# Optimization experiments

Hardware: AMD Instinct MI355X
Metric: run time of the kernel (lower is better)

The kernel has to match this reference:

```python
import jax, jax.numpy as jnp
import numpy as np

N_HEAD = 16

def _rope_cache(dim, T):
    # matches precompute_rope_cache: angles = outer(pos, 1/theta^(2i/dim))
    pos = jnp.arange(T, dtype=jnp.float32)
    freq = 1.0 / (10000.0 ** (jnp.arange(0, dim, 2, dtype=jnp.float32) / dim))
    ang = pos[:, None] * freq[None, :]  # (T, dim//2)
    return jnp.cos(ang), jnp.sin(ang)

def _apply_rope(x, cos, sin):
    # x: (B, H, T, hs). Faithful to the (nonstandard, roll-based) torch apply_rope,
    # including the reassignment of x_rot before it is used for x_pass.
    x_rot, x_pass = x[..., ::2], x[..., 1::2]
    c = cos[None, None]  # (1,1,T,hs//2)
    s = sin[None, None]
    new_rot = x_rot * c - jnp.roll(x_pass, 1, axis=-1) * s
    new_pass = x_pass * c + jnp.roll(new_rot, -1, axis=-1) * s
    return jnp.stack([new_rot, new_pass], axis=-1).reshape(x.shape)

def setup_inputs() -> dict:
    key = jax.random.key(0)
    k1, k2, k3 = jax.random.split(key, 3)
    B, T, C = 2, 2048, 1024
    x = jax.random.normal(k1, (B, T, C), dtype=jnp.float32)
    w_attn = jax.random.normal(k2, (3 * C, C), dtype=jnp.float32) * 0.02
    w_proj = jax.random.normal(k3, (C, C), dtype=jnp.float32) * 0.02
    return {"x": x, "w_attn": w_attn, "w_proj": w_proj}

def reference(x, w_attn, w_proj):
    B, T, C = x.shape
    H = N_HEAD
    hs = C // H
    qkv = jnp.einsum('btc,dc->btd', x, w_attn)  # fused QKV projection (no bias)
    q, k, v = jnp.split(qkv, 3, axis=-1)
    def heads(t):
        return t.reshape(B, T, H, hs).transpose(0, 2, 1, 3)  # (B,H,T,hs)
    q, k, v = heads(q), heads(k), heads(v)
    cos, sin = _rope_cache(hs, T)
    q = _apply_rope(q, cos, sin)
    k = _apply_rope(k, cos, sin)
    scores = jnp.einsum('bhqd,bhkd->bhqk', q, k) / jnp.sqrt(jnp.float32(hs))
    causal = jnp.tril(jnp.ones((T, T), dtype=bool))
    scores = jnp.where(causal[None, None], scores, -jnp.inf)
    att = jax.nn.softmax(scores, axis=-1)
    y = jnp.einsum('bhqk,bhkd->bhqd', att, v)
    y = y.transpose(0, 2, 1, 3).reshape(B, T, C)
    return jnp.einsum('btc,dc->btd', y, w_proj)
```

## Files before the change

kernel.cpp:

```cpp
#include <hip/hip_runtime.h>

#define T_SEQ 2048
#define NHEAD 16
#define HS 64

typedef __bf16 bf16x8 __attribute__((ext_vector_type(8)));
typedef float f32x4 __attribute__((ext_vector_type(4)));
typedef short short4v __attribute__((ext_vector_type(4)));

__device__ __forceinline__ unsigned short f2bf(float f) {
  union { float f; unsigned int u; } v; v.f = f;
  return (unsigned short)((v.u + 0x7fffu + ((v.u >> 16) & 1u)) >> 16);
}
__device__ __forceinline__ float bf2f(unsigned short h) {
  union { unsigned int u; float f; } v; v.u = ((unsigned int)h) << 16;
  return v.f;
}
__device__ __forceinline__ bf16x8 ld_bf8(const unsigned short* p) {
  return *(const bf16x8*)p;
}
__device__ __forceinline__ void st_bf8(unsigned short* p, bf16x8 v) {
  *(bf16x8*)p = v;
}
__device__ __forceinline__ bf16x8 cvt8(float4 a, float4 b) {
  bf16x8 r;
  r[0] = (__bf16)a.x; r[1] = (__bf16)a.y; r[2] = (__bf16)a.z; r[3] = (__bf16)a.w;
  r[4] = (__bf16)b.x; r[5] = (__bf16)b.y; r[6] = (__bf16)b.z; r[7] = (__bf16)b.w;
  return r;
}

__global__ __launch_bounds__(256, 2) void gemm_bt(
    const void* __restrict__ Av, const void* __restrict__ Bv,
    float* __restrict__ Cout,
    unsigned short* __restrict__ qb, unsigned short* __restrict__ kb,
    unsigned short* __restrict__ vtb,
    int M, int N, int K, int af32, int bf32, int mode) {
  __shared__ unsigned short As[128 * 64];
  __shared__ unsigned short Bs[128 * 64];
  const int tid = threadIdx.x;
  const int wid = tid >> 6, lane = tid & 63;
  const int quad = lane >> 4, l16 = lane & 15;
  const int m0 = blockIdx.y * 128, n0 = blockIdx.x * 128;
  const int wm = (wid >> 1) * 64, wn = (wid & 1) * 64;
  const int row_in = tid >> 3;
  const int col_in = (tid & 7) * 8;
  const float* Agf = (const float*)Av + (size_t)(m0 + row_in) * K + col_in;
  const float* Bgf = (const float*)Bv + (size_t)(n0 + row_in) * K + col_in;
  const unsigned short* Agh = (const unsigned short*)Av + (size_t)(m0 + row_in) * K + col_in;
  const unsigned short* Bgh = (const unsigned short*)Bv + (size_t)(n0 + row_in) * K + col_in;
  f32x4 acc[4][4] = {};
  const int nkt = K >> 6;
  for (int kt = 0; kt < nkt; ++kt) {
    bf16x8 as8[4], bs8[4];
    if (af32) {
      #pragma unroll
      for (int j = 0; j < 4; ++j) {
        const float* p = Agf + (size_t)j * 32 * K + kt * 64;
        as8[j] = cvt8(*(const float4*)p, *(const float4*)(p + 4));
      }
    } else {
      #pragma unroll
      for (int j = 0; j < 4; ++j)
        as8[j] = ld_bf8(Agh + (size_t)j * 32 * K + kt * 64);
    }
    if (bf32) {
      #pragma unroll
      for (int j = 0; j < 4; ++j) {
        const float* p = Bgf + (size_t)j * 32 * K + kt * 64;
        bs8[j] = cvt8(*(const float4*)p, *(const float4*)(p + 4));
      }
    } else {
      #pragma unroll
      for (int j = 0; j < 4; ++j)
        bs8[j] = ld_bf8(Bgh + (size_t)j * 32 * K + kt * 64);
    }
    __syncthreads();
    #pragma unroll
    for (int j = 0; j < 4; ++j) {
      st_bf8(&As[(j * 32 + row_in) * 64 + col_in], as8[j]);
      st_bf8(&Bs[(j * 32 + row_in) * 64 + col_in], bs8[j]);
    }
    __syncthreads();
    #pragma unroll
    for (int ks = 0; ks < 2; ++ks) {
      bf16x8 af[4], bfr[4];
      #pragma unroll
      for (int mt = 0; mt < 4; ++mt)
        af[mt] = ld_bf8(&As[(wm + mt * 16 + l16) * 64 + ks * 32 + quad * 8]);
      #pragma unroll
      for (int nt = 0; nt < 4; ++nt)
        bfr[nt] = ld_bf8(&Bs[(wn + nt * 16 + l16) * 64 + ks * 32 + quad * 8]);
      #pragma unroll
      for (int mt = 0; mt < 4; ++mt)
        #pragma unroll
        for (int nt = 0; nt < 4; ++nt)
          acc[mt][nt] = __builtin_amdgcn_mfma_f32_16x16x32_bf16(af[mt], bfr[nt], acc[mt][nt], 0, 0, 0);
    }
  }
  #pragma unroll
  for (int mt = 0; mt < 4; ++mt) {
    #pragma unroll
    for (int nt = 0; nt < 4; ++nt) {
      const int n = n0 + wn + nt * 16 + l16;
      #pragma unroll
      for (int r = 0; r < 4; ++r) {
        const int m = m0 + wm + mt * 16 + quad * 4 + r;
        if (mode == 0) {
          Cout[(size_t)m * N + n] = acc[mt][nt][r];
        } else {
          const unsigned short val = f2bf(acc[mt][nt][r]);
          const int b = m >> 11, t = m & (T_SEQ - 1);
          const int which = n >> 10, c = n & 1023;
          const int h = c >> 6, d = c & 63;
          const int bh = b * NHEAD + h;
          if (which == 0)      qb[((size_t)bh * T_SEQ + t) * HS + d] = val;
          else if (which == 1) kb[((size_t)bh * T_SEQ + t) * HS + d] = val;
          else                 vtb[((size_t)bh * HS + d) * T_SEQ + t] = val;
        }
      }
    }
  }
}

__global__ __launch_bounds__(256) void cvtbuf(const float* __restrict__ src,
                                              unsigned short* __restrict__ dst, int n) {
  const int i = (blockIdx.x * 256 + threadIdx.x) * 4;
  if (i < n) {
    const float4 v = *(const float4*)(src + i);
    ushort4 o;
    o.x = f2bf(v.x); o.y = f2bf(v.y); o.z = f2bf(v.z); o.w = f2bf(v.w);
    *(ushort4*)(dst + i) = o;
  }
}

__global__ __launch_bounds__(256, 1) void rope(unsigned short* __restrict__ qb,
                                               unsigned short* __restrict__ kb) {
  const int idx = blockIdx.x * 256 + threadIdx.x;
  const bool isq = idx < 65536;
  const float qs = isq ? 0.125f : 1.0f;
  unsigned short* buf = (isq ? qb : kb) + (size_t)(idx & 65535) * HS;
  const int t = idx & (T_SEQ - 1);
  float x[64];
  #pragma unroll
  for (int j = 0; j < 64; ++j) x[j] = bf2f(buf[j]);
  __asm__ volatile("" ::: "memory");
  float c[32], s[32], er[32];
  #pragma unroll
  for (int i = 0; i < 32; ++i) {
    const float ang = (float)t * exp2f(-0.41524101186092029f * (float)i);
    c[i] = cosf(ang); s[i] = sinf(ang);
  }
  #pragma unroll
  for (int i = 0; i < 32; ++i)
    er[i] = x[2 * i] * c[i] - x[(2 * i + 63) & 63] * s[i];
  #pragma unroll
  for (int i = 0; i < 32; ++i) {
    const float ep = x[2 * i + 1] * c[i] + er[(i + 1) & 31] * s[i];
    buf[2 * i]     = f2bf(er[i] * qs);
    buf[2 * i + 1] = f2bf(ep * qs);
  }
}

__global__ __launch_bounds__(64, 4) void attn(
    const unsigned short* __restrict__ qb, const unsigned short* __restrict__ kb,
    const unsigned short* __restrict__ vt, unsigned short* __restrict__ yb) {
  const int u = blockIdx.x;
  const int qi = 127 - (u >> 5);
  const int bh = u & 31;
  const int q0 = qi * 16;
  const int lane = threadIdx.x & 63;
  const int quad = lane >> 4, l16 = lane & 15;

  const unsigned short* qptr = qb + ((size_t)bh * T_SEQ + q0 + l16) * HS;
  const bf16x8 bq0 = ld_bf8(qptr + quad * 8);
  const bf16x8 bq1 = ld_bf8(qptr + 32 + quad * 8);

  f32x4 O[4] = {};
  float m_i = -1e30f, l_i = 0.f;

  const unsigned short* kbase = kb + (size_t)bh * T_SEQ * HS;
  const unsigned short* vbase = vt + (size_t)bh * HS * T_SEQ;
  const int nfull = (q0 >= 63) ? (((q0 - 63) >> 6) + 1) : 0;

  auto pass_body = [&](int k0, bool masked) {
    bf16x8 ak[4][2];
    #pragma unroll
    for (int t = 0; t < 4; ++t) {
      const unsigned short* kp = kbase + (size_t)(k0 + t * 16 + l16) * HS;
      ak[t][0] = ld_bf8(kp + quad * 8);
      ak[t][1] = ld_bf8(kp + 32 + quad * 8);
    }
    short4v vf[4][4];
    #pragma unroll
    for (int t = 0; t < 4; ++t)
      #pragma unroll
      for (int dg = 0; dg < 4; ++dg)
        vf[t][dg] = *(const short4v*)(vbase + (size_t)(dg * 16 + l16) * T_SEQ + k0 + t * 16 + quad * 4);
    f32x4 S[4] = {};
    #pragma unroll
    for (int t = 0; t < 4; ++t) {
      S[t] = __builtin_amdgcn_mfma_f32_16x16x32_bf16(ak[t][0], bq0, S[t], 0, 0, 0);
      S[t] = __builtin_amdgcn_mfma_f32_16x16x32_bf16(ak[t][1], bq1, S[t], 0, 0, 0);
    }
    float sv[16];
    #pragma unroll
    for (int t = 0; t < 4; ++t)
      #pragma unroll
      for (int r = 0; r < 4; ++r) {
        float v = S[t][r];
        if (masked) v = (k0 + t * 16 + quad * 4 + r <= q0 + l16) ? v : -1e30f;
        sv[t * 4 + r] = v;
      }
    float tm = sv[0];
    #pragma unroll
    for (int i = 1; i < 16; ++i) tm = fmaxf(tm, sv[i]);
    tm = fmaxf(tm, __shfl_xor(tm, 16, 64));
    tm = fmaxf(tm, __shfl_xor(tm, 32, 64));
    const float mnew = fmaxf(m_i, tm);
    const float alpha = __expf(m_i - mnew);
    float p[16], rs = 0.f;
    #pragma unroll
    for (int i = 0; i < 16; ++i) { p[i] = __expf(sv[i] - mnew); rs += p[i]; }
    rs += __shfl_xor(rs, 16, 64);
    rs += __shfl_xor(rs, 32, 64);
    l_i = l_i * alpha + rs;
    m_i = mnew;
    short4v pa[4];
    #pragma unroll
    for (int t = 0; t < 4; ++t) {
      short4v f;
      f[0] = (short)f2bf(p[t * 4 + 0]); f[1] = (short)f2bf(p[t * 4 + 1]);
      f[2] = (short)f2bf(p[t * 4 + 2]); f[3] = (short)f2bf(p[t * 4 + 3]);
      pa[t] = f;
    }
    float aD[4];
    #pragma unroll
    for (int r = 0; r < 4; ++r) aD[r] = __shfl(alpha, quad * 4 + r, 64);
    #pragma unroll
    for (int dg = 0; dg < 4; ++dg)
      #pragma unroll
      for (int r = 0; r < 4; ++r) O[dg][r] *= aD[r];
    #pragma unroll
    for (int t = 0; t < 4; ++t)
      #pragma unroll
      for (int dg = 0; dg < 4; ++dg)
        O[dg] = __builtin_amdgcn_mfma_f32_16x16x16bf16_1k(pa[t], vf[t][dg], O[dg], 0, 0, 0);
  };

  for (int k0 = 0; k0 < nfull * 64; k0 += 64) pass_body(k0, false);
  pass_body(nfull * 64, true);

  const int b = bh >> 4, h = bh & 15;
  float inv[4];
  #pragma unroll
  for (int r = 0; r < 4; ++r)
    inv[r] = 1.0f / fmaxf(__shfl(l_i, quad * 4 + r, 64), 1e-30f);
  #pragma unroll
  for (int r = 0; r < 4; ++r) {
    const int row = q0 + quad * 4 + r;
    #pragma unroll
    for (int dg = 0; dg < 4; ++dg)
      yb[((size_t)b * T_SEQ + row) * 1024 + h * HS + dg * 16 + l16] = f2bf(O[dg][r] * inv[r]);
  }
}

extern "C" void kernel_launch(void* const* d_in, const int* in_sizes, int n_in,
                              void* d_out, int out_size, void* d_ws, size_t ws_size,
                              hipStream_t stream) {
  const float* x      = (const float*)d_in[0];
  const float* w_attn = (const float*)d_in[1];
  const float* w_proj = (const float*)d_in[2];
  float* out = (float*)d_out;
  unsigned short* qb = (unsigned short*)d_ws;
  unsigned short* kb = qb + (size_t)4194304;
  unsigned short* vt = kb + (size_t)4194304;
  unsigned short* yb = vt + (size_t)4194304;

  if (ws_size >= (size_t)50331648 + (size_t)2097152) {
    unsigned short* xb  = yb + (size_t)4194304;
    unsigned short* wab = xb + (size_t)4194304;
    unsigned short* wpb = wab + (size_t)3145728;
    cvtbuf<<<dim3(4096), 256, 0, stream>>>(x, xb, 4194304);
    cvtbuf<<<dim3(3072), 256, 0, stream>>>(w_attn, wab, 3145728);
    cvtbuf<<<dim3(1024), 256, 0, stream>>>(w_proj, wpb, 1048576);
    gemm_bt<<<dim3(24, 32), 256, 0, stream>>>(xb, wab, nullptr, qb, kb, vt,
                                              4096, 3072, 1024, 0, 0, 1);
    rope<<<dim3(512), 256, 0, stream>>>(qb, kb);
    attn<<<dim3(4096), 64, 0, stream>>>(qb, kb, vt, yb);
    gemm_bt<<<dim3(8, 32), 256, 0, stream>>>(yb, wpb, out, nullptr, nullptr, nullptr,
                                             4096, 1024, 1024, 0, 0, 0);
  } else {
    gemm_bt<<<dim3(24, 32), 256, 0, stream>>>(x, w_attn, nullptr, qb, kb, vt,
                                              4096, 3072, 1024, 1, 1, 1);
    rope<<<dim3(512), 256, 0, stream>>>(qb, kb);
    attn<<<dim3(4096), 64, 0, stream>>>(qb, kb, vt, yb);
    gemm_bt<<<dim3(8, 32), 256, 0, stream>>>(yb, w_proj, out, nullptr, nullptr, nullptr,
                                             4096, 1024, 1024, 0, 1, 0);
  }
}
```

Measured before the change: 353.6 us.

## Split attention key loop across four waves per block with LDS merge

The attention kernel now launches 256 threads per block and distributes the 64-key tiles round-robin across four waves. Each wave keeps its own online-softmax state, and the partial results are merged in shared memory before wave 0 writes the normalized output. This is meant to shorten the serial per-block key loop for long causal rows and add latency hiding. In exchange it adds shared-memory use, a block barrier and merge work, and waves sit idle for short query rows.

```diff
diff --git a/kernel.cpp b/kernel.cpp
--- a/kernel.cpp
+++ b/kernel.cpp
@@ -161,13 +161,16 @@
   }
 }
 
-__global__ __launch_bounds__(64, 4) void attn(
+__global__ __launch_bounds__(256, 4) void attn(
     const unsigned short* __restrict__ qb, const unsigned short* __restrict__ kb,
     const unsigned short* __restrict__ vt, unsigned short* __restrict__ yb) {
+  __shared__ float Om[4][16][64];
+  __shared__ float Ml[4][2][16];
   const int u = blockIdx.x;
   const int qi = 127 - (u >> 5);
   const int bh = u & 31;
   const int q0 = qi * 16;
+  const int wid = threadIdx.x >> 6;
   const int lane = threadIdx.x & 63;
   const int quad = lane >> 4, l16 = lane & 15;
 
@@ -180,9 +183,11 @@
 
   const unsigned short* kbase = kb + (size_t)bh * T_SEQ * HS;
   const unsigned short* vbase = vt + (size_t)bh * HS * T_SEQ;
-  const int nfull = (q0 >= 63) ? (((q0 - 63) >> 6) + 1) : 0;
-
-  auto pass_body = [&](int k0, bool masked) {
+  const int P = (q0 + 16 + 63) >> 6;
+
+  for (int p = wid; p < P; p += 4) {
+    const int k0 = p * 64;
+    const bool masked = (p == P - 1);
     bf16x8 ak[4][2];
     #pragma unroll
     for (int t = 0; t < 4; ++t) {
@@ -218,9 +223,9 @@
     tm = fmaxf(tm, __shfl_xor(tm, 32, 64));
     const float mnew = fmaxf(m_i, tm);
     const float alpha = __expf(m_i - mnew);
-    float p[16], rs = 0.f;
-    #pragma unroll
-    for (int i = 0; i < 16; ++i) { p[i] = __expf(sv[i] - mnew); rs += p[i]; }
+    float p16[16], rs = 0.f;
+    #pragma unroll
+    for (int i = 0; i < 16; ++i) { p16[i] = __expf(sv[i] - mnew); rs += p16[i]; }
     rs += __shfl_xor(rs, 16, 64);
     rs += __shfl_xor(rs, 32, 64);
     l_i = l_i * alpha + rs;
@@ -229,8 +234,8 @@
     #pragma unroll
     for (int t = 0; t < 4; ++t) {
       short4v f;
-      f[0] = (short)f2bf(p[t * 4 + 0]); f[1] = (short)f2bf(p[t * 4 + 1]);
-      f[2] = (short)f2bf(p[t * 4 + 2]); f[3] = (short)f2bf(p[t * 4 + 3]);
+      f[0] = (short)f2bf(p16[t * 4 + 0]); f[1] = (short)f2bf(p16[t * 4 + 1]);
+      f[2] = (short)f2bf(p16[t * 4 + 2]); f[3] = (short)f2bf(p16[t * 4 + 3]);
       pa[t] = f;
     }
     float aD[4];
@@ -245,22 +250,36 @@
       #pragma unroll
       for (int dg = 0; dg < 4; ++dg)
         O[dg] = __builtin_amdgcn_mfma_f32_16x16x16bf16_1k(pa[t], vf[t][dg], O[dg], 0, 0, 0);
-  };
-
-  for (int k0 = 0; k0 < nfull * 64; k0 += 64) pass_body(k0, false);
-  pass_body(nfull * 64, true);
+  }
+
+  if (quad == 0) { Ml[wid][0][l16] = m_i; Ml[wid][1][l16] = l_i; }
+  #pragma unroll
+  for (int dg = 0; dg < 4; ++dg)
+    #pragma unroll
+    for (int r = 0; r < 4; ++r)
+      Om[wid][quad * 4 + r][dg * 16 + l16] = O[dg][r];
+  __syncthreads();
+  if (wid != 0) return;
 
   const int b = bh >> 4, h = bh & 15;
-  float inv[4];
-  #pragma unroll
-  for (int r = 0; r < 4; ++r)
-    inv[r] = 1.0f / fmaxf(__shfl(l_i, quad * 4 + r, 64), 1e-30f);
   #pragma unroll
   for (int r = 0; r < 4; ++r) {
-    const int row = q0 + quad * 4 + r;
-    #pragma unroll
-    for (int dg = 0; dg < 4; ++dg)
-      yb[((size_t)b * T_SEQ + row) * 1024 + h * HS + dg * 16 + l16] = f2bf(O[dg][r] * inv[r]);
+    const int row = quad * 4 + r;
+    float mw[4];
+    #pragma unroll
+    for (int w = 0; w < 4; ++w) mw[w] = Ml[w][0][row];
+    const float ms = fmaxf(fmaxf(mw[0], mw[1]), fmaxf(mw[2], mw[3]));
+    float fw[4], ls = 0.f;
+    #pragma unroll
+    for (int w = 0; w < 4; ++w) { fw[w] = __expf(mw[w] - ms); ls += fw[w] * Ml[w][1][row]; }
+    const float inv = 1.0f / fmaxf(ls, 1e-30f);
+    #pragma unroll
+    for (int dg = 0; dg < 4; ++dg) {
+      float ov = 0.f;
+      #pragma unroll
+      for (int w = 0; w < 4; ++w) ov += Om[w][row][dg * 16 + l16] * fw[w];
+      yb[((size_t)b * T_SEQ + q0 + row) * 1024 + h * HS + dg * 16 + l16] = f2bf(ov * inv);
+    }
   }
 }
 
@@ -286,14 +305,14 @@
     gemm_bt<<<dim3(24, 32), 256, 0, stream>>>(xb, wab, nullptr, qb, kb, vt,
                                               4096, 3072, 1024, 0, 0, 1);
     rope<<<dim3(512), 256, 0, stream>>>(qb, kb);
-    attn<<<dim3(4096), 64, 0, stream>>>(qb, kb, vt, yb);
+    attn<<<dim3(4096), 256, 0, stream>>>(qb, kb, vt, yb);
     gemm_bt<<<dim3(8, 32), 256, 0, stream>>>(yb, wpb, out, nullptr, nullptr, nullptr,
                                              4096, 1024, 1024, 0, 0, 0);
   } else {
     gemm_bt<<<dim3(24, 32), 256, 0, stream>>>(x, w_attn, nullptr, qb, kb, vt,
                                               4096, 3072, 1024, 1, 1, 1);
     rope<<<dim3(512), 256, 0, stream>>>(qb, kb);
-    attn<<<dim3(4096), 64, 0, stream>>>(qb, kb, vt, yb);
+    attn<<<dim3(4096), 256, 0, stream>>>(qb, kb, vt, yb);
     gemm_bt<<<dim3(8, 32), 256, 0, stream>>>(yb, w_proj, out, nullptr, nullptr, nullptr,
                                              4096, 1024, 1024, 0, 1, 0);
   }
```

Result: no change. 352.7 us (-0.2%).
